# Performance work log

Hardware: AMD Instinct MI355X
Metric: run time of the kernel (lower is better)

Reference implementation:

```python
import jax, jax.numpy as jnp
import numpy as np

N_NODES = 100000


def gcn_conv(x, edge_index, W, b):
    """PyG GCNConv: add self-loops, symmetric deg^{-1/2} A deg^{-1/2} aggregation.

    x: [N, Fin], edge_index: [2, E] int (row 0 = src, row 1 = dst).
    Transform first (Fin -> Fout), then gather-normalize-scatter at Fout.
    """
    n = x.shape[0]
    loops = jnp.arange(n, dtype=edge_index.dtype)
    src = jnp.concatenate([edge_index[0], loops])
    dst = jnp.concatenate([edge_index[1], loops])
    # in-degree with self-loops (all edge weights = 1)
    deg = jax.ops.segment_sum(jnp.ones_like(dst, dtype=x.dtype), dst, num_segments=n)
    dinv = jax.lax.rsqrt(deg)  # deg >= 1 thanks to self-loops
    norm = dinv[src] * dinv[dst]  # [E+N]
    h = x @ W  # [N, Fout] dense transform before sparse aggregation
    msgs = norm[:, None] * h[src]  # gather + normalize
    out = jax.ops.segment_sum(msgs, dst, num_segments=n)  # scatter-add
    return out + b


def setup_inputs() -> dict:
    key = jax.random.key(0)
    ks = jax.random.split(key, 8)
    N, E, Fin, H, C = N_NODES, 1600000, 256, 64, 11
    x = jax.random.normal(ks[0], (N, Fin), dtype=jnp.float32)
    edge_index = jax.random.randint(ks[1], (2, E), 0, N, dtype=jnp.int64)
    s1 = 1.0 / np.sqrt(Fin)
    s2 = 1.0 / np.sqrt(H)
    W1 = jax.random.uniform(ks[2], (Fin, H), jnp.float32, -s1, s1)
    b1 = jnp.zeros((H,), jnp.float32)
    W2 = jax.random.uniform(ks[3], (H, H), jnp.float32, -s2, s2)
    b2 = jnp.zeros((H,), jnp.float32)
    Wfc = jax.random.uniform(ks[4], (H, C), jnp.float32, -s2, s2)
    bfc = jax.random.uniform(ks[5], (C,), jnp.float32, -s2, s2)
    return {"x": x, "edge_index": edge_index, "W1": W1, "b1": b1,
            "W2": W2, "b2": b2, "Wfc": Wfc, "bfc": bfc}


def reference(x, edge_index, W1, b1, W2, b2, Wfc, bfc):
    h = jax.nn.relu(gcn_conv(x, edge_index, W1, b1))
    h = jax.nn.relu(gcn_conv(h, edge_index, W2, b2))
    return h @ Wfc + bfc  # [N, 11]
```

## Files before the change

kernel.cpp:

```cpp
#include <hip/hip_runtime.h>
#include <hip/hip_fp16.h>

#define NFEAT 64
#define SCAN_CHUNK 2048

typedef _Float16 half8 __attribute__((ext_vector_type(8)));
typedef float f32x4 __attribute__((ext_vector_type(4)));

__device__ __forceinline__ void gll16(const float* g, float* l) {
    __builtin_amdgcn_global_load_lds(
        (const __attribute__((address_space(1))) unsigned int*)g,
        (__attribute__((address_space(3))) unsigned int*)l, 16, 0, 0);
}

__device__ __forceinline__ __half2 bch(unsigned int u) {
    return __builtin_bit_cast(__half2, u);
}

__global__ void k_zero(int* p, int n) {
    int i = blockIdx.x * 256 + threadIdx.x;
    if (i < n) p[i] = 0;
}

__global__ void k_count(const int* __restrict__ ei, int* __restrict__ counts,
                        int* __restrict__ rank, int E) {
    int e = blockIdx.x * 256 + threadIdx.x;
    if (e < E) rank[e] = atomicAdd(&counts[ei[(size_t)E + e]], 1);
}

__global__ void k_dinv(const int* __restrict__ counts, float* dinv, int n) {
    int i = blockIdx.x * 256 + threadIdx.x;
    if (i < n) dinv[i] = rsqrtf((float)(counts[i] + 1));
}

__global__ __launch_bounds__(256) void k_scan_block(const int* __restrict__ counts,
                                                    int* __restrict__ bsums, int n) {
    __shared__ int red[256];
    int tid = threadIdx.x;
    int base = blockIdx.x * SCAN_CHUNK + tid * 8;
    int s = 0;
#pragma unroll
    for (int i = 0; i < 8; ++i) {
        int idx = base + i;
        s += (idx < n) ? counts[idx] : 0;
    }
    red[tid] = s;
    __syncthreads();
    for (int off = 128; off; off >>= 1) {
        if (tid < off) red[tid] += red[tid + off];
        __syncthreads();
    }
    if (tid == 0) bsums[blockIdx.x] = red[0];
}

__global__ void k_scan_sums(int* bsums, int nb) {
    __shared__ int ts[64];
    int tid = threadIdx.x;
    if (tid < 64) ts[tid] = (tid < nb) ? bsums[tid] : 0;
    __syncthreads();
    if (tid == 0) {
        int run = 0;
        for (int i = 0; i < nb; ++i) { int t = ts[i]; ts[i] = run; run += t; }
    }
    __syncthreads();
    if (tid < nb) bsums[tid] = ts[tid];
}

__global__ __launch_bounds__(256) void k_scan_final(const int* __restrict__ counts,
                                                    const int* __restrict__ bsums,
                                                    int* __restrict__ rowptr, int n) {
    __shared__ int ts[256];
    int tid = threadIdx.x;
    int base0 = blockIdx.x * SCAN_CHUNK + tid * 8;
    int v[8], c[8];
    int s = 0;
#pragma unroll
    for (int i = 0; i < 8; ++i) {
        int idx = base0 + i;
        c[i] = (idx < n) ? counts[idx] : 0;
        v[i] = s;
        s += c[i];
    }
    ts[tid] = s;
    __syncthreads();
    for (int off = 1; off < 256; off <<= 1) {
        int t = (tid >= off) ? ts[tid - off] : 0;
        __syncthreads();
        if (tid >= off) ts[tid] += t;
        __syncthreads();
    }
    int texcl = ts[tid] - s;
    int base = bsums[blockIdx.x] + texcl;
#pragma unroll
    for (int i = 0; i < 8; ++i) {
        int idx = base0 + i;
        if (idx < n) {
            int val = base + v[i];
            rowptr[idx] = val;
            if (idx == n - 1) rowptr[n] = val + c[i];
        }
    }
}

__global__ void k_build(const int* __restrict__ ei, const int* __restrict__ rank,
                        const int* __restrict__ rowptr, int* __restrict__ col, int E) {
    int e = blockIdx.x * 256 + threadIdx.x;
    if (e >= E) return;
    int src = ei[e];
    int dst = ei[(size_t)E + e];
    col[rowptr[dst] + rank[e]] = src;
}

__global__ void k_cvtW(const float* __restrict__ W, __half* __restrict__ Wt, int K) {
    int idx = blockIdx.x * 256 + threadIdx.x;
    if (idx >= 64 * K) return;
    int n = idx / K;
    int k = idx % K;
    Wt[idx] = __float2half(W[(size_t)k * NFEAT + n]);
}

template<int K>
__global__ __launch_bounds__(256) void k_gemm(
    const float* __restrict__ A, const __half* __restrict__ Wt,
    const float* __restrict__ dinv, __half* __restrict__ H, int M)
{
    const int BM = 128, BK = 32;
    const int WROW = K + 8;
    __shared__ float As[2 * BM * BK];
    __shared__ __half Wlds[64 * WROW];

    int tid = threadIdx.x;
    int w = tid >> 6, lane = tid & 63;
    int q = lane >> 4, n16 = lane & 15;
    int m0 = blockIdx.x * BM;

    auto stage = [&](int k0, int buf) {
#pragma unroll
        for (int rep = 0; rep < 4; ++rep) {
            int cb = (w * 4 + rep) * 64;
            int s = cb + lane;
            int m = s >> 3;
            int kk = (s & 7) ^ (m & 7);
            int row = m0 + m; if (row > M - 1) row = M - 1;
            gll16(A + (size_t)row * K + k0 + kk * 4,
                  &As[buf * (BM * BK) + cb * 4]);
        }
    };

    stage(0, 0);

    for (int idx = tid; idx < 64 * (K / 8); idx += 256) {
        int row = idx / (K / 8);
        int c = idx % (K / 8);
        *(uint4*)&Wlds[row * WROW + c * 8] = *(const uint4*)&Wt[(size_t)row * K + c * 8];
    }

    f32x4 acc[2][4];
#pragma unroll
    for (int t = 0; t < 2; ++t)
#pragma unroll
        for (int nt = 0; nt < 4; ++nt) acc[t][nt] = (f32x4)(0.f);

    const int T = K / BK;
    for (int kt = 0; kt < T; ++kt) {
        __syncthreads();
        if (kt + 1 < T) stage((kt + 1) * BK, (kt + 1) & 1);
        const float* As_ = &As[(kt & 1) * (BM * BK)];

        half8 ahi[2], alo[2];
#pragma unroll
        for (int t = 0; t < 2; ++t) {
            int ml = w * 32 + t * 16 + n16;
            int e0 = (2 * q) ^ (ml & 7);
            int e1 = (2 * q + 1) ^ (ml & 7);
            float4 f0 = *(const float4*)&As_[(ml * 8 + e0) * 4];
            float4 f1 = *(const float4*)&As_[(ml * 8 + e1) * 4];
            float fv[8] = {f0.x, f0.y, f0.z, f0.w, f1.x, f1.y, f1.z, f1.w};
#pragma unroll
            for (int j = 0; j < 8; ++j) {
                _Float16 hi = (_Float16)fv[j];
                ahi[t][j] = hi;
                alo[t][j] = (_Float16)(fv[j] - (float)hi);
            }
        }
#pragma unroll
        for (int nt = 0; nt < 4; ++nt) {
            uint4 u = *(const uint4*)&Wlds[(nt * 16 + n16) * WROW + kt * BK + q * 8];
            half8 b = __builtin_bit_cast(half8, u);
            acc[0][nt] = __builtin_amdgcn_mfma_f32_16x16x32_f16(ahi[0], b, acc[0][nt], 0, 0, 0);
            acc[0][nt] = __builtin_amdgcn_mfma_f32_16x16x32_f16(alo[0], b, acc[0][nt], 0, 0, 0);
            acc[1][nt] = __builtin_amdgcn_mfma_f32_16x16x32_f16(ahi[1], b, acc[1][nt], 0, 0, 0);
            acc[1][nt] = __builtin_amdgcn_mfma_f32_16x16x32_f16(alo[1], b, acc[1][nt], 0, 0, 0);
        }
        __syncthreads();
    }

#pragma unroll
    for (int t = 0; t < 2; ++t) {
#pragma unroll
        for (int reg = 0; reg < 4; ++reg) {
            int row = m0 + w * 32 + t * 16 + q * 4 + reg;
            if (row < M) {
                float di = dinv[row];
#pragma unroll
                for (int nt = 0; nt < 4; ++nt)
                    H[(size_t)row * NFEAT + nt * 16 + n16] =
                        __float2half(di * acc[t][nt][reg]);
            }
        }
    }
}

template<bool FC>
__global__ __launch_bounds__(256) void k_aggr(
    const __half* __restrict__ h, const int* __restrict__ rowptr,
    const int* __restrict__ col, const float* __restrict__ dinv,
    const float* __restrict__ bias, const float* __restrict__ Wfc,
    const float* __restrict__ bfc, float* __restrict__ out, int n)
{
    __shared__ float Wl[NFEAT * 11 + 11];
    int tid = threadIdx.x;
    if (FC) {
        for (int i = tid; i < NFEAT * 11; i += 256) Wl[i] = Wfc[i];
        if (tid < 11) Wl[NFEAT * 11 + tid] = bfc[tid];
        __syncthreads();
    }
    int lane = tid & 63;
    int li = lane & 7;
    int fi = li << 3;
    int r = blockIdx.x * 32 + ((tid >> 6) << 3) + (lane >> 3);
    bool valid = r < n;

    int beg = 0, end = 0;
    if (valid) { beg = rowptr[r]; end = rowptr[r + 1]; }

    const __half* hp = h + fi;
    auto ld = [&](int src) { return *(const uint4*)(hp + (size_t)src * NFEAT); };

    float a0 = 0.f, a1 = 0.f, a2 = 0.f, a3 = 0.f,
          a4 = 0.f, a5 = 0.f, a6 = 0.f, a7 = 0.f;
    auto addu = [&](uint4 u) {
        float2 f0 = __half22float2(bch(u.x));
        float2 f1 = __half22float2(bch(u.y));
        float2 f2 = __half22float2(bch(u.z));
        float2 f3 = __half22float2(bch(u.w));
        a0 += f0.x; a1 += f0.y; a2 += f1.x; a3 += f1.y;
        a4 += f2.x; a5 += f2.y; a6 += f3.x; a7 += f3.y;
    };

    if (valid) addu(ld(r));
    int j = beg;
    for (; j + 1 < end; j += 2) {
        uint4 u0 = ld(col[j]);
        uint4 u1 = ld(col[j + 1]);
        uint4 s;
        s.x = __builtin_bit_cast(unsigned int, __hadd2(bch(u0.x), bch(u1.x)));
        s.y = __builtin_bit_cast(unsigned int, __hadd2(bch(u0.y), bch(u1.y)));
        s.z = __builtin_bit_cast(unsigned int, __hadd2(bch(u0.z), bch(u1.z)));
        s.w = __builtin_bit_cast(unsigned int, __hadd2(bch(u0.w), bch(u1.w)));
        addu(s);
    }
    if (j < end) addu(ld(col[j]));

    if (!valid) return;
    float di = dinv[r];
    float t0 = fmaxf(bias[fi + 0] + di * a0, 0.f);
    float t1 = fmaxf(bias[fi + 1] + di * a1, 0.f);
    float t2 = fmaxf(bias[fi + 2] + di * a2, 0.f);
    float t3 = fmaxf(bias[fi + 3] + di * a3, 0.f);
    float t4 = fmaxf(bias[fi + 4] + di * a4, 0.f);
    float t5 = fmaxf(bias[fi + 5] + di * a5, 0.f);
    float t6 = fmaxf(bias[fi + 6] + di * a6, 0.f);
    float t7 = fmaxf(bias[fi + 7] + di * a7, 0.f);

    if (!FC) {
        float4 lo = make_float4(t0, t1, t2, t3);
        float4 hi = make_float4(t4, t5, t6, t7);
        float* op = out + (size_t)r * NFEAT + fi;
        *(float4*)op = lo;
        *(float4*)(op + 4) = hi;
    } else {
#pragma unroll
        for (int c = 0; c < 11; ++c) {
            const float* wc = &Wl[fi * 11 + c];
            float p = t0 * wc[0] + t1 * wc[11] + t2 * wc[22] + t3 * wc[33]
                    + t4 * wc[44] + t5 * wc[55] + t6 * wc[66] + t7 * wc[77];
            p += __shfl_xor(p, 1, 64);
            p += __shfl_xor(p, 2, 64);
            p += __shfl_xor(p, 4, 64);
            if (li == 0) out[(size_t)r * 11 + c] = p + Wl[NFEAT * 11 + c];
        }
    }
}

extern "C" void kernel_launch(void* const* d_in, const int* in_sizes, int n_in,
                              void* d_out, int out_size, void* d_ws, size_t ws_size,
                              hipStream_t stream) {
    const float* x   = (const float*)d_in[0];
    const int*   ei  = (const int*)d_in[1];
    const float* W1  = (const float*)d_in[2];
    const float* b1  = (const float*)d_in[3];
    const float* W2  = (const float*)d_in[4];
    const float* b2  = (const float*)d_in[5];
    const float* Wfc = (const float*)d_in[6];
    const float* bfc = (const float*)d_in[7];
    float* out = (float*)d_out;

    const int Fin = 256;
    int N = in_sizes[0] / Fin;
    int E = in_sizes[1] / 2;

    char* ws = (char*)d_ws;
    size_t off = 0;
    auto alloc = [&](size_t bytes) { void* p = ws + off; off = (off + bytes + 255) & ~(size_t)255; return p; };
    int*    counts = (int*)   alloc((size_t)N * 4);
    int*    rowptr = (int*)   alloc((size_t)(N + 1) * 4);
    float*  dinv   = (float*) alloc((size_t)N * 4);
    int*    bsums  = (int*)   alloc(64 * 4);
    int*    rank   = (int*)   alloc((size_t)E * 4);
    int*    col    = (int*)   alloc((size_t)E * 4);
    __half* Wt1    = (__half*)alloc((size_t)64 * 256 * 2);
    __half* Wt2    = (__half*)alloc((size_t)64 * 64 * 2);
    __half* A      = (__half*)alloc((size_t)N * NFEAT * 2);
    float*  B      = (float*) alloc((size_t)N * NFEAT * 4);

    int gN = (N + 255) / 256;
    int gE = (E + 255) / 256;
    int gb = (N + 127) / 128;
    int gA = (N + 31) / 32;
    int nb = (N + SCAN_CHUNK - 1) / SCAN_CHUNK;

    k_zero<<<gN, 256, 0, stream>>>(counts, N);
    k_count<<<gE, 256, 0, stream>>>(ei, counts, rank, E);
    k_cvtW<<<(64 * 256 + 255) / 256, 256, 0, stream>>>(W1, Wt1, 256);
    k_cvtW<<<(64 * 64 + 255) / 256, 256, 0, stream>>>(W2, Wt2, 64);
    k_dinv<<<gN, 256, 0, stream>>>(counts, dinv, N);
    k_scan_block<<<nb, 256, 0, stream>>>(counts, bsums, N);
    k_scan_sums<<<1, 64, 0, stream>>>(bsums, nb);
    k_scan_final<<<nb, 256, 0, stream>>>(counts, bsums, rowptr, N);
    k_build<<<gE, 256, 0, stream>>>(ei, rank, rowptr, col, E);

    k_gemm<256><<<gb, 256, 0, stream>>>(x, Wt1, dinv, A, N);
    k_aggr<false><<<gA, 256, 0, stream>>>(A, rowptr, col, dinv, b1, nullptr, nullptr, B, N);

    k_gemm<64><<<gb, 256, 0, stream>>>(B, Wt2, dinv, A, N);
    k_aggr<true><<<gA, 256, 0, stream>>>(A, rowptr, col, dinv, b2, Wfc, bfc, out, N);
}
```

Before: 386.7 us.

## Overlap edge degree counting with first GEMM and merge graph-build kernels

The edge-degree atomic counting now runs inside the first GEMM launch: two of every three blocks count edges using vectorized int4 loads, and the third does GEMM tiles. This lets the atomics overlap the dense transform. Because dinv is not known yet at that point, the first GEMM writes an unscaled result. A later combined kernel, run alongside the CSR column build, rescales that fp16 output in place. The dinv computation is also merged into the scan-block kernel, and a memset replaces the zero kernel. The cost is an extra read and write pass over the hidden matrix and a second fp16 rounding step.

```diff
diff --git a/kernel.cpp b/kernel.cpp
--- a/kernel.cpp
+++ b/kernel.cpp
@@ -15,100 +15,6 @@
 
 __device__ __forceinline__ __half2 bch(unsigned int u) {
     return __builtin_bit_cast(__half2, u);
-}
-
-__global__ void k_zero(int* p, int n) {
-    int i = blockIdx.x * 256 + threadIdx.x;
-    if (i < n) p[i] = 0;
-}
-
-__global__ void k_count(const int* __restrict__ ei, int* __restrict__ counts,
-                        int* __restrict__ rank, int E) {
-    int e = blockIdx.x * 256 + threadIdx.x;
-    if (e < E) rank[e] = atomicAdd(&counts[ei[(size_t)E + e]], 1);
-}
-
-__global__ void k_dinv(const int* __restrict__ counts, float* dinv, int n) {
-    int i = blockIdx.x * 256 + threadIdx.x;
-    if (i < n) dinv[i] = rsqrtf((float)(counts[i] + 1));
-}
-
-__global__ __launch_bounds__(256) void k_scan_block(const int* __restrict__ counts,
-                                                    int* __restrict__ bsums, int n) {
-    __shared__ int red[256];
-    int tid = threadIdx.x;
-    int base = blockIdx.x * SCAN_CHUNK + tid * 8;
-    int s = 0;
-#pragma unroll
-    for (int i = 0; i < 8; ++i) {
-        int idx = base + i;
-        s += (idx < n) ? counts[idx] : 0;
-    }
-    red[tid] = s;
-    __syncthreads();
-    for (int off = 128; off; off >>= 1) {
-        if (tid < off) red[tid] += red[tid + off];
-        __syncthreads();
-    }
-    if (tid == 0) bsums[blockIdx.x] = red[0];
-}
-
-__global__ void k_scan_sums(int* bsums, int nb) {
-    __shared__ int ts[64];
-    int tid = threadIdx.x;
-    if (tid < 64) ts[tid] = (tid < nb) ? bsums[tid] : 0;
-    __syncthreads();
-    if (tid == 0) {
-        int run = 0;
-        for (int i = 0; i < nb; ++i) { int t = ts[i]; ts[i] = run; run += t; }
-    }
-    __syncthreads();
-    if (tid < nb) bsums[tid] = ts[tid];
-}
-
-__global__ __launch_bounds__(256) void k_scan_final(const int* __restrict__ counts,
-                                                    const int* __restrict__ bsums,
-                                                    int* __restrict__ rowptr, int n) {
-    __shared__ int ts[256];
-    int tid = threadIdx.x;
-    int base0 = blockIdx.x * SCAN_CHUNK + tid * 8;
-    int v[8], c[8];
-    int s = 0;
-#pragma unroll
-    for (int i = 0; i < 8; ++i) {
-        int idx = base0 + i;
-        c[i] = (idx < n) ? counts[idx] : 0;
-        v[i] = s;
-        s += c[i];
-    }
-    ts[tid] = s;
-    __syncthreads();
-    for (int off = 1; off < 256; off <<= 1) {
-        int t = (tid >= off) ? ts[tid - off] : 0;
-        __syncthreads();
-        if (tid >= off) ts[tid] += t;
-        __syncthreads();
-    }
-    int texcl = ts[tid] - s;
-    int base = bsums[blockIdx.x] + texcl;
-#pragma unroll
-    for (int i = 0; i < 8; ++i) {
-        int idx = base0 + i;
-        if (idx < n) {
-            int val = base + v[i];
-            rowptr[idx] = val;
-            if (idx == n - 1) rowptr[n] = val + c[i];
-        }
-    }
-}
-
-__global__ void k_build(const int* __restrict__ ei, const int* __restrict__ rank,
-                        const int* __restrict__ rowptr, int* __restrict__ col, int E) {
-    int e = blockIdx.x * 256 + threadIdx.x;
-    if (e >= E) return;
-    int src = ei[e];
-    int dst = ei[(size_t)E + e];
-    col[rowptr[dst] + rank[e]] = src;
 }
 
 __global__ void k_cvtW(const float* __restrict__ W, __half* __restrict__ Wt, int K) {
@@ -119,20 +25,46 @@
     Wt[idx] = __float2half(W[(size_t)k * NFEAT + n]);
 }
 
-template<int K>
-__global__ __launch_bounds__(256) void k_gemm(
+template<int K, bool SCALE, bool CNT>
+__global__ __launch_bounds__(256) void k_gemm_x(
     const float* __restrict__ A, const __half* __restrict__ Wt,
-    const float* __restrict__ dinv, __half* __restrict__ H, int M)
+    const float* __restrict__ dinv, __half* __restrict__ H, int M,
+    const int* __restrict__ eiDst, int* __restrict__ counts,
+    int* __restrict__ rank, int E)
 {
+    int tid = threadIdx.x;
+    int gemmIdx;
+    if (CNT) {
+        int bid = blockIdx.x;
+        if (bid % 3 != 2) {
+            int cIdx = bid - (bid + 1) / 3;
+            int t = (cIdx * 256 + tid) * 4;
+            if (t + 3 < E) {
+                int4 d = *(const int4*)(eiDst + t);
+                int r0 = atomicAdd(&counts[d.x], 1);
+                int r1 = atomicAdd(&counts[d.y], 1);
+                int r2 = atomicAdd(&counts[d.z], 1);
+                int r3 = atomicAdd(&counts[d.w], 1);
+                *(int4*)(rank + t) = make_int4(r0, r1, r2, r3);
+            } else {
+                for (int e = t; e < E; ++e)
+                    rank[e] = atomicAdd(&counts[eiDst[e]], 1);
+            }
+            return;
+        }
+        gemmIdx = bid / 3;
+    } else {
+        gemmIdx = blockIdx.x;
+    }
+
     const int BM = 128, BK = 32;
     const int WROW = K + 8;
     __shared__ float As[2 * BM * BK];
     __shared__ __half Wlds[64 * WROW];
 
-    int tid = threadIdx.x;
     int w = tid >> 6, lane = tid & 63;
     int q = lane >> 4, n16 = lane & 15;
-    int m0 = blockIdx.x * BM;
+    int m0 = gemmIdx * BM;
 
     auto stage = [&](int k0, int buf) {
 #pragma unroll
@@ -201,13 +133,118 @@
         for (int reg = 0; reg < 4; ++reg) {
             int row = m0 + w * 32 + t * 16 + q * 4 + reg;
             if (row < M) {
-                float di = dinv[row];
+                float di = SCALE ? dinv[row] : 1.0f;
 #pragma unroll
                 for (int nt = 0; nt < 4; ++nt)
                     H[(size_t)row * NFEAT + nt * 16 + n16] =
                         __float2half(di * acc[t][nt][reg]);
             }
         }
+    }
+}
+
+__global__ __launch_bounds__(256) void k_dinv_scan(
+    const int* __restrict__ counts, int* __restrict__ bsums,
+    float* __restrict__ dinv, int n, int nbScan)
+{
+    __shared__ int red[256];
+    int bid = blockIdx.x;
+    int tid = threadIdx.x;
+    if (bid < nbScan) {
+        int base = bid * SCAN_CHUNK + tid * 8;
+        int s = 0;
+#pragma unroll
+        for (int i = 0; i < 8; ++i) {
+            int idx = base + i;
+            s += (idx < n) ? counts[idx] : 0;
+        }
+        red[tid] = s;
+        __syncthreads();
+        for (int off = 128; off; off >>= 1) {
+            if (tid < off) red[tid] += red[tid + off];
+            __syncthreads();
+        }
+        if (tid == 0) bsums[bid] = red[0];
+    } else {
+        int i = (bid - nbScan) * 256 + tid;
+        if (i < n) dinv[i] = rsqrtf((float)(counts[i] + 1));
+    }
+}
+
+__global__ void k_scan_sums(int* bsums, int nb) {
+    __shared__ int ts[64];
+    int tid = threadIdx.x;
+    if (tid < 64) ts[tid] = (tid < nb) ? bsums[tid] : 0;
+    __syncthreads();
+    if (tid == 0) {
+        int run = 0;
+        for (int i = 0; i < nb; ++i) { int t = ts[i]; ts[i] = run; run += t; }
+    }
+    __syncthreads();
+    if (tid < nb) bsums[tid] = ts[tid];
+}
+
+__global__ __launch_bounds__(256) void k_scan_final(const int* __restrict__ counts,
+                                                    const int* __restrict__ bsums,
+                                                    int* __restrict__ rowptr, int n) {
+    __shared__ int ts[256];
+    int tid = threadIdx.x;
+    int base0 = blockIdx.x * SCAN_CHUNK + tid * 8;
+    int v[8], c[8];
+    int s = 0;
+#pragma unroll
+    for (int i = 0; i < 8; ++i) {
+        int idx = base0 + i;
+        c[i] = (idx < n) ? counts[idx] : 0;
+        v[i] = s;
+        s += c[i];
+    }
+    ts[tid] = s;
+    __syncthreads();
+    for (int off = 1; off < 256; off <<= 1) {
+        int t = (tid >= off) ? ts[tid - off] : 0;
+        __syncthreads();
+        if (tid >= off) ts[tid] += t;
+        __syncthreads();
+    }
+    int texcl = ts[tid] - s;
+    int base = bsums[blockIdx.x] + texcl;
+#pragma unroll
+    for (int i = 0; i < 8; ++i) {
+        int idx = base0 + i;
+        if (idx < n) {
+            int val = base + v[i];
+            rowptr[idx] = val;
+            if (idx == n - 1) rowptr[n] = val + c[i];
+        }
+    }
+}
+
+__global__ __launch_bounds__(256) void k_build_scale(
+    const int* __restrict__ ei, const int* __restrict__ rank,
+    const int* __restrict__ rowptr, int* __restrict__ col, int E,
+    __half* __restrict__ A, const float* __restrict__ dinv, int N, int gE)
+{
+    int bid = blockIdx.x;
+    if (bid < gE) {
+        int e = bid * 256 + threadIdx.x;
+        if (e >= E) return;
+        int src = ei[e];
+        int dst = ei[(size_t)E + e];
+        col[rowptr[dst] + rank[e]] = src;
+    } else {
+        int i = (bid - gE) * 256 + threadIdx.x;
+        if (i >= N * 8) return;
+        float di = dinv[i >> 3];
+        uint4* p = (uint4*)A + i;
+        uint4 u = *p;
+        auto sc = [&](unsigned int x) {
+            float2 f = __half22float2(bch(x));
+            return __builtin_bit_cast(unsigned int,
+                   __float22half2_rn(make_float2(f.x * di, f.y * di)));
+        };
+        u.x = sc(u.x); u.y = sc(u.y); u.z = sc(u.z); u.w = sc(u.w);
+        *p = u;
     }
 }
 
@@ -324,25 +361,29 @@
     __half* A      = (__half*)alloc((size_t)N * NFEAT * 2);
     float*  B      = (float*) alloc((size_t)N * NFEAT * 4);
 
-    int gN = (N + 255) / 256;
     int gE = (E + 255) / 256;
     int gb = (N + 127) / 128;
     int gA = (N + 31) / 32;
+    int gS = (N * 8 + 255) / 256;
     int nb = (N + SCAN_CHUNK - 1) / SCAN_CHUNK;
-
-    k_zero<<<gN, 256, 0, stream>>>(counts, N);
-    k_count<<<gE, 256, 0, stream>>>(ei, counts, rank, E);
+    int gN = (N + 255) / 256;
+
+    hipMemsetAsync(counts, 0, (size_t)N * 4, stream);
     k_cvtW<<<(64 * 256 + 255) / 256, 256, 0, stream>>>(W1, Wt1, 256);
     k_cvtW<<<(64 * 64 + 255) / 256, 256, 0, stream>>>(W2, Wt2, 64);
-    k_dinv<<<gN, 256, 0, stream>>>(counts, dinv, N);
-    k_scan_block<<<nb, 256, 0, stream>>>(counts, bsums, N);
+
+    k_gemm_x<256, false, true><<<gb * 3, 256, 0, stream>>>(
+        x, Wt1, nullptr, A, N, ei + E, counts, rank, E);
+
+    k_dinv_scan<<<nb + gN, 256, 0, stream>>>(counts, bsums, dinv, N, nb);
     k_scan_sums<<<1, 64, 0, stream>>>(bsums, nb);
     k_scan_final<<<nb, 256, 0, stream>>>(counts, bsums, rowptr, N);
-    k_build<<<gE, 256, 0, stream>>>(ei, rank, rowptr, col, E);
-
-    k_gemm<256><<<gb, 256, 0, stream>>>(x, Wt1, dinv, A, N);
+
+    k_build_scale<<<gE + gS, 256, 0, stream>>>(ei, rank, rowptr, col, E, A, dinv, N, gE);
+
     k_aggr<false><<<gA, 256, 0, stream>>>(A, rowptr, col, dinv, b1, nullptr, nullptr, B, N);
 
-    k_gemm<64><<<gb, 256, 0, stream>>>(B, Wt2, dinv, A, N);
+    k_gemm_x<64, true, false><<<gb, 256, 0, stream>>>(
+        B, Wt2, dinv, A, N, nullptr, nullptr, nullptr, 0);
     k_aggr<true><<<gA, 256, 0, stream>>>(A, rowptr, col, dinv, b2, Wfc, bfc, out, N);
 }
```

Measured after the change: 354.9 us. 8.2% less time.
